# Performance work log

Hardware: AMD Instinct MI355X
Metric: run time of the kernel (lower is better)

The kernel has to match this reference:

```python
import jax, jax.numpy as jnp
import numpy as np

H, DH, DM = 8, 128, 1024          # n_head, d_head, d_model (n_head*d_head == d_model)
SLEN, BSZ = 256, 64               # slen <= 256 forced by pi0[:, :l]
SCALE = 1.0 / DH ** 0.5
LN_EPS = 1e-5


def setup_inputs() -> dict:
    key = jax.random.key(0)
    k0, k1, k2, k3 = jax.random.split(key, 4)
    h = jax.random.normal(k0, (SLEN, BSZ, DM), jnp.float32)
    W_qkv = jax.random.normal(k1, (H * 4 * DH, DM), jnp.float32) * (DM ** -0.5)
    W_o = jax.random.normal(k2, (DM, H * DH), jnp.float32) * ((H * DH) ** -0.5)
    pi0 = jax.random.uniform(k3, (H, 256), jnp.float32)
    ln_gamma = jnp.ones((DM,), jnp.float32)
    ln_beta = jnp.zeros((DM,), jnp.float32)
    return {"h": h, "W_qkv": W_qkv, "W_o": W_o, "pi0": pi0,
            "ln_gamma": ln_gamma, "ln_beta": ln_beta}


def _phi(x):
    # elu(x)+1 feature map, then L1-normalize over the feature dim
    x = jax.nn.elu(x) + 1.0
    return x / jnp.sum(x, axis=-1, keepdims=True)


def _causal_linear_attn(q, k, v):
    # fast_weight_sum: out_t = sum_{s<=t} (q_t . k_s) v_s  (zero initial fast weights)
    # q,k,v: [b,h,l,d]
    l = q.shape[2]
    scores = jnp.einsum('bhld,bhsd->bhls', q, k)
    mask = jnp.tril(jnp.ones((l, l), dtype=bool))
    scores = jnp.where(mask, scores, jnp.zeros((), scores.dtype))
    return jnp.einsum('bhls,bhsd->bhld', scores, v)


def reference(h, W_qkv, W_o, pi0, ln_gamma, ln_beta):
    l, b, _ = h.shape
    # qkv projection: [l,b,H,4*DH] -> q, k1, k2, v (update_mode='rbf2keys')
    qkv = jnp.einsum('lbm,nm->lbn', h, W_qkv).reshape(l, b, H, 4 * DH)
    q, k1, k2, v = jnp.split(qkv, 4, axis=-1)
    # permute to [b, H, l, d]
    q = _phi(jnp.transpose(q, (1, 2, 0, 3)))
    k1 = _phi(jnp.transpose(k1, (1, 2, 0, 3)))
    k2 = _phi(jnp.transpose(k2, (1, 2, 0, 3)))
    v = jnp.transpose(v, (1, 2, 0, 3))
    # two fast-weight sums (skip_attn_normalization=True path)
    lo1 = _causal_linear_attn(q, k1, v)
    lo2 = _causal_linear_attn(q, k2, v)
    pi = jnp.clip(pi0, 0.0, 1.0)[None, :, :l, None]          # [1,H,l,1]
    layer_out = SCALE * (lo1 * pi + lo2 * (1.0 - pi))         # [b,H,l,d]
    # [b,H,l,d] -> [l,b,H*d]
    layer_out = jnp.transpose(layer_out, (2, 0, 1, 3)).reshape(l, b, H * DH)
    attn_out = jnp.einsum('lbn,mn->lbm', layer_out, W_o)
    # post-LN residual (pre_lnorm=False, dropout=0)
    x = h + attn_out
    mu = jnp.mean(x, axis=-1, keepdims=True)
    var = jnp.mean((x - mu) ** 2, axis=-1, keepdims=True)
    return ln_gamma * (x - mu) / jnp.sqrt(var + LN_EPS) + ln_beta
```

## Files before the change

kernel.cpp:

```cpp
#include <hip/hip_runtime.h>

#define H_     8
#define DM_    1024
#define NQKV_  4096
#define ROWS_  16384
#define PAIRS_ 512
#define SCALE_ 0.08838834764831845f
#define LN_EPS_ 1e-5f

typedef __attribute__((ext_vector_type(8))) short short8;
typedef __attribute__((ext_vector_type(4))) float floatx4;

__device__ __forceinline__ float b2f(unsigned short u) {
  union { unsigned int i; float f; } v; v.i = ((unsigned int)u) << 16; return v.f;
}
__device__ __forceinline__ unsigned short f2b(float f) {
  union { unsigned int i; float f; } v; v.f = f;
  unsigned int b = v.i;
  b += 0x7FFFu + ((b >> 16) & 1u);
  return (unsigned short)(b >> 16);
}

__device__ __forceinline__ void stage_async(const unsigned short* __restrict__ g,
                                            size_t ld, unsigned short* s, int tid) {
#pragma unroll
  for (int p = 0; p < 4; ++p) {
    int idx = p * 256 + tid;
    int r = idx >> 3, j = idx & 7;
    int cg = j ^ (r & 7);
    __builtin_amdgcn_global_load_lds(
        (const __attribute__((address_space(1))) unsigned int*)(g + (size_t)r * ld + cg * 8),
        (__attribute__((address_space(3))) unsigned int*)(s + (size_t)idx * 8),
        16, 0, 0);
  }
}
__device__ __forceinline__ short8 lds_frag(const unsigned short* s, int row, int cg) {
  return *(const short8*)(s + row * 64 + ((cg ^ (row & 7)) << 3));
}

__global__ __launch_bounds__(256) void cvt_all(const float* __restrict__ h,
                                               const float* __restrict__ wq,
                                               const float* __restrict__ wo,
                                               unsigned short* __restrict__ hb,
                                               unsigned short* __restrict__ wqb,
                                               unsigned short* __restrict__ wob) {
  int i = blockIdx.x * 256 + threadIdx.x;
  const float* src; unsigned short* dst; int off;
  if (i < 2097152)      { src = h;  dst = hb;  off = i; }
  else if (i < 2621440) { src = wq; dst = wqb; off = i - 2097152; }
  else                  { src = wo; dst = wob; off = i - 2621440; }
  const float4* s4 = (const float4*)(src + (size_t)off * 8);
  float4 v0 = s4[0], v1 = s4[1];
  union { short8 v; unsigned short u[8]; } pk;
  pk.u[0] = f2b(v0.x); pk.u[1] = f2b(v0.y); pk.u[2] = f2b(v0.z); pk.u[3] = f2b(v0.w);
  pk.u[4] = f2b(v1.x); pk.u[5] = f2b(v1.y); pk.u[6] = f2b(v1.z); pk.u[7] = f2b(v1.w);
  *(short8*)(dst + (size_t)off * 8) = pk.v;
}

__global__ __launch_bounds__(256, 2) void qkv_gemm(const unsigned short* __restrict__ A,
                                                   const unsigned short* __restrict__ B,
                                                   unsigned short* __restrict__ QKV) {
  __shared__ alignas(16) unsigned short Sh[34816];
  unsigned short* As = Sh;
  unsigned short* Bs = Sh + 8192;
  int tid = threadIdx.x;
  int lane = tid & 63, wid = tid >> 6;
  int wm = wid >> 1, wn = wid & 1;
  int quad = lane >> 4, l16 = lane & 15;
  int n0 = blockIdx.x * 256;
  int hh = n0 >> 9, part0 = (n0 >> 7) & 3;
  int bb = blockIdx.y & 63, lhalf = blockIdx.y >> 6;

  const unsigned short* Ab = A + ((size_t)(lhalf * 128) * 64 + bb) * DM_;
  const size_t lda = (size_t)64 * DM_;
  const unsigned short* Bb = B + (size_t)n0 * DM_;

  floatx4 acc[4][8];
#pragma unroll
  for (int i = 0; i < 4; ++i)
#pragma unroll
    for (int j = 0; j < 8; ++j)
#pragma unroll
      for (int r = 0; r < 4; ++r) acc[i][j][r] = 0.f;

  for (int kt = 0; kt < DM_; kt += 64) {
    stage_async(Ab + kt, lda, As, tid);
    stage_async(Bb + kt, DM_, Bs, tid);
    stage_async(Bb + (size_t)128 * DM_ + kt, DM_, Bs + 8192, tid);
    __syncthreads();
#pragma unroll
    for (int kk = 0; kk < 2; ++kk) {
      short8 af[4], bfv[8];
#pragma unroll
      for (int mt = 0; mt < 4; ++mt)
        af[mt] = lds_frag(As, wm * 64 + mt * 16 + l16, kk * 4 + quad);
#pragma unroll
      for (int nt = 0; nt < 8; ++nt)
        bfv[nt] = lds_frag(Bs, wn * 128 + nt * 16 + l16, kk * 4 + quad);
#pragma unroll
      for (int mt = 0; mt < 4; ++mt)
#pragma unroll
        for (int nt = 0; nt < 8; ++nt)
          acc[mt][nt] = __builtin_amdgcn_mfma_f32_16x16x32_bf16(af[mt], bfv[nt], acc[mt][nt], 0, 0, 0);
    }
    __syncthreads();
  }

  int mypart = part0 + wn;
  unsigned short* T = Sh + wn * 17408;
  if (mypart < 3) {
    float rsum[4][4];
#pragma unroll
    for (int mt = 0; mt < 4; ++mt)
#pragma unroll
      for (int r = 0; r < 4; ++r) rsum[mt][r] = 0.f;
#pragma unroll
    for (int mt = 0; mt < 4; ++mt)
#pragma unroll
      for (int nt = 0; nt < 8; ++nt)
#pragma unroll
        for (int r = 0; r < 4; ++r) {
          float x = acc[mt][nt][r];
          float f = x > 0.f ? x + 1.f : __expf(x);
          acc[mt][nt][r] = f;
          rsum[mt][r] += f;
        }
#pragma unroll
    for (int off = 1; off < 16; off <<= 1)
#pragma unroll
      for (int mt = 0; mt < 4; ++mt)
#pragma unroll
        for (int r = 0; r < 4; ++r)
          rsum[mt][r] += __shfl_xor(rsum[mt][r], off);
#pragma unroll
    for (int mt = 0; mt < 4; ++mt)
#pragma unroll
      for (int r = 0; r < 4; ++r) {
        float inv = 1.f / rsum[mt][r];
        int rl = wm * 64 + mt * 16 + quad * 4 + r;
#pragma unroll
        for (int nt = 0; nt < 8; ++nt)
          T[rl * 136 + nt * 16 + l16] = f2b(acc[mt][nt][r] * inv);
      }
  } else {
#pragma unroll
    for (int mt = 0; mt < 4; ++mt)
#pragma unroll
      for (int nt = 0; nt < 8; ++nt)
#pragma unroll
        for (int r = 0; r < 4; ++r) {
          int l = wm * 64 + mt * 16 + quad * 4 + r;
          int d = nt * 16 + l16;
          T[d * 136 + l] = f2b(acc[mt][nt][r]);
        }
  }
  __syncthreads();

  int c = tid & 15, g = tid >> 4;
#pragma unroll
  for (int half = 0; half < 2; ++half) {
    int part = part0 + half;
    const unsigned short* Th = Sh + half * 17408;
    if (part < 3) {
      unsigned short* P = QKV + (size_t)part * 16777216;
      size_t base = ((size_t)((bb * 8 + hh) * 256 + lhalf * 128)) * 128;
#pragma unroll
      for (int j = 0; j < 8; ++j) {
        int rr = j * 16 + g;
        *(short8*)(P + base + rr * 128 + c * 8) = *(const short8*)(Th + rr * 136 + c * 8);
      }
    } else {
      unsigned short* Vt = QKV + (size_t)3 * 16777216;
#pragma unroll
      for (int j = 0; j < 8; ++j) {
        int d = j * 16 + g;
        size_t gb = ((size_t)((bb * 8 + hh) * 128 + d)) * 256 + lhalf * 128 + c * 8;
        *(short8*)(Vt + gb) = *(const short8*)(Th + d * 136 + c * 8);
      }
    }
  }
}

__global__ __launch_bounds__(256) void scores_kernel(const unsigned short* __restrict__ QKV,
                                                     const float* __restrict__ pi0,
                                                     unsigned short* __restrict__ S) {
  __shared__ alignas(16) unsigned short Sh[24576];
  __shared__ float pis[128];
  unsigned short* As  = Sh;
  unsigned short* Bs1 = Sh + 8192;
  unsigned short* Bs2 = Sh + 16384;
  int p = blockIdx.z;
  int hh = p & 7;
  int tid = threadIdx.x;
  int lane = tid & 63, wid = tid >> 6;
  int wm = wid >> 1, wn = wid & 1;
  int quad = lane >> 4, l16 = lane & 15;
  int tix = blockIdx.x;
  int m0 = (tix >= 1) ? 128 : 0;
  int n0 = (tix == 2) ? 128 : 0;
  if (tid < 128) {
    float pv = pi0[hh * 256 + m0 + tid];
    pis[tid] = fminf(fmaxf(pv, 0.f), 1.f);
  }
  const unsigned short* Qb  = QKV + (size_t)p * 32768 + (size_t)m0 * 128;
  const unsigned short* K1b = QKV + 16777216     + (size_t)p * 32768 + (size_t)n0 * 128;
  const unsigned short* K2b = QKV + 2 * 16777216 + (size_t)p * 32768 + (size_t)n0 * 128;

  floatx4 acc1[4][4], acc2[4][4];
#pragma unroll
  for (int i = 0; i < 4; ++i)
#pragma unroll
    for (int j = 0; j < 4; ++j)
#pragma unroll
      for (int r = 0; r < 4; ++r) { acc1[i][j][r] = 0.f; acc2[i][j][r] = 0.f; }

  for (int kt = 0; kt < 128; kt += 64) {
    stage_async(Qb + kt, 128, As, tid);
    stage_async(K1b + kt, 128, Bs1, tid);
    stage_async(K2b + kt, 128, Bs2, tid);
    __syncthreads();
#pragma unroll
    for (int kk = 0; kk < 2; ++kk) {
      short8 af[4], b1[4], b2v[4];
#pragma unroll
      for (int mt = 0; mt < 4; ++mt)
        af[mt] = lds_frag(As, wm * 64 + mt * 16 + l16, kk * 4 + quad);
#pragma unroll
      for (int nt = 0; nt < 4; ++nt) {
        b1[nt]  = lds_frag(Bs1, wn * 64 + nt * 16 + l16, kk * 4 + quad);
        b2v[nt] = lds_frag(Bs2, wn * 64 + nt * 16 + l16, kk * 4 + quad);
      }
#pragma unroll
      for (int mt = 0; mt < 4; ++mt)
#pragma unroll
        for (int nt = 0; nt < 4; ++nt) {
          acc1[mt][nt] = __builtin_amdgcn_mfma_f32_16x16x32_bf16(af[mt], b1[nt],  acc1[mt][nt], 0, 0, 0);
          acc2[mt][nt] = __builtin_amdgcn_mfma_f32_16x16x32_bf16(af[mt], b2v[nt], acc2[mt][nt], 0, 0, 0);
        }
    }
    __syncthreads();
  }
#pragma unroll
  for (int mt = 0; mt < 4; ++mt)
#pragma unroll
    for (int nt = 0; nt < 4; ++nt)
#pragma unroll
      for (int r = 0; r < 4; ++r) {
        int tl = wm * 64 + mt * 16 + quad * 4 + r;
        int sl = wn * 64 + nt * 16 + l16;
        float pv = pis[tl];
        float v = (n0 + sl <= m0 + tl) ? (pv * acc1[mt][nt][r] + (1.f - pv) * acc2[mt][nt][r]) : 0.f;
        Sh[tl * 136 + sl] = f2b(v);
      }
  __syncthreads();
  int c = tid & 15, g = tid >> 4;
#pragma unroll
  for (int j = 0; j < 8; ++j) {
    int r = j * 16 + g;
    size_t gb = (size_t)p * 65536 + (size_t)(m0 + r) * 256 + n0 + c * 8;
    *(short8*)(S + gb) = *(const short8*)(Sh + r * 136 + c * 8);
  }
}

__global__ __launch_bounds__(256, 4) void pv_kernel(const unsigned short* __restrict__ S,
                                                    const unsigned short* __restrict__ Vt,
                                                    unsigned short* __restrict__ LO) {
  __shared__ alignas(16) unsigned short Sh[17408];
  unsigned short* As = Sh;
  unsigned short* Bs = Sh + 8192;
  int p = blockIdx.z;
  int b = p >> 3, hh = p & 7;
  int tid = threadIdx.x;
  int lane = tid & 63, wid = tid >> 6;
  int wm = wid >> 1, wn = wid & 1;
  int quad = lane >> 4, l16 = lane & 15;
  int m0 = blockIdx.y * 128;
  int kEnd = (blockIdx.y == 0) ? 128 : 256;
  const unsigned short* Ab = S  + (size_t)p * 65536 + (size_t)m0 * 256;
  const unsigned short* Bb = Vt + (size_t)p * 32768;

  floatx4 acc[4][4];
#pragma unroll
  for (int i = 0; i < 4; ++i)
#pragma unroll
    for (int j = 0; j < 4; ++j)
#pragma unroll
      for (int r = 0; r < 4; ++r) acc[i][j][r] = 0.f;

  for (int kt = 0; kt < kEnd; kt += 64) {
    stage_async(Ab + kt, 256, As, tid);
    stage_async(Bb + kt, 256, Bs, tid);
    __syncthreads();
#pragma unroll
    for (int kk = 0; kk < 2; ++kk) {
      short8 af[4], bfv[4];
#pragma unroll
      for (int mt = 0; mt < 4; ++mt)
        af[mt] = lds_frag(As, wm * 64 + mt * 16 + l16, kk * 4 + quad);
#pragma unroll
      for (int nt = 0; nt < 4; ++nt)
        bfv[nt] = lds_frag(Bs, wn * 64 + nt * 16 + l16, kk * 4 + quad);
#pragma unroll
      for (int mt = 0; mt < 4; ++mt)
#pragma unroll
        for (int nt = 0; nt < 4; ++nt)
          acc[mt][nt] = __builtin_amdgcn_mfma_f32_16x16x32_bf16(af[mt], bfv[nt], acc[mt][nt], 0, 0, 0);
    }
    __syncthreads();
  }
#pragma unroll
  for (int mt = 0; mt < 4; ++mt)
#pragma unroll
    for (int nt = 0; nt < 4; ++nt)
#pragma unroll
      for (int r = 0; r < 4; ++r) {
        int tl = wm * 64 + mt * 16 + quad * 4 + r;
        int d = wn * 64 + nt * 16 + l16;
        Sh[tl * 136 + d] = f2b(SCALE_ * acc[mt][nt][r]);
      }
  __syncthreads();
  int c = tid & 15, g = tid >> 4;
#pragma unroll
  for (int j = 0; j < 8; ++j) {
    int r = j * 16 + g;
    int t = m0 + r;
    size_t gb = ((size_t)t * 64 + b) * 1024 + hh * 128 + c * 8;
    *(short8*)(LO + gb) = *(const short8*)(Sh + r * 136 + c * 8);
  }
}

__global__ __launch_bounds__(256, 4) void wo_gemm(const unsigned short* __restrict__ A,
                                                  const unsigned short* __restrict__ B,
                                                  const float* __restrict__ hin,
                                                  float* __restrict__ X) {
  __shared__ alignas(16) unsigned short As[128 * 64], Bs[128 * 64];
  int tid = threadIdx.x;
  int lane = tid & 63, wid = tid >> 6;
  int wm = wid >> 1, wn = wid & 1;
  int quad = lane >> 4, l16 = lane & 15;
  int m0 = blockIdx.y * 128, n0 = blockIdx.x * 128;
  const unsigned short* Ab = A + (size_t)m0 * DM_;
  const unsigned short* Bb = B + (size_t)n0 * DM_;

  floatx4 acc[4][4];
#pragma unroll
  for (int i = 0; i < 4; ++i)
#pragma unroll
    for (int j = 0; j < 4; ++j)
#pragma unroll
      for (int r = 0; r < 4; ++r) acc[i][j][r] = 0.f;

  for (int kt = 0; kt < DM_; kt += 64) {
    stage_async(Ab + kt, DM_, As, tid);
    stage_async(Bb + kt, DM_, Bs, tid);
    __syncthreads();
#pragma unroll
    for (int kk = 0; kk < 2; ++kk) {
      short8 af[4], bfv[4];
#pragma unroll
      for (int mt = 0; mt < 4; ++mt)
        af[mt] = lds_frag(As, wm * 64 + mt * 16 + l16, kk * 4 + quad);
#pragma unroll
      for (int nt = 0; nt < 4; ++nt)
        bfv[nt] = lds_frag(Bs, wn * 64 + nt * 16 + l16, kk * 4 + quad);
#pragma unroll
      for (int mt = 0; mt < 4; ++mt)
#pragma unroll
        for (int nt = 0; nt < 4; ++nt)
          acc[mt][nt] = __builtin_amdgcn_mfma_f32_16x16x32_bf16(af[mt], bfv[nt], acc[mt][nt], 0, 0, 0);
    }
    __syncthreads();
  }
#pragma unroll
  for (int mt = 0; mt < 4; ++mt)
#pragma unroll
    for (int nt = 0; nt < 4; ++nt)
#pragma unroll
      for (int r = 0; r < 4; ++r) {
        int row = m0 + wm * 64 + mt * 16 + quad * 4 + r;
        int col = n0 + wn * 64 + nt * 16 + l16;
        size_t idx = (size_t)row * DM_ + col;
        X[idx] = acc[mt][nt][r] + hin[idx];
      }
}

__global__ __launch_bounds__(256) void ln_kernel(float* __restrict__ X,
                                                 const float* __restrict__ gamma,
                                                 const float* __restrict__ beta) {
  int row = blockIdx.x;
  int tid = threadIdx.x;
  float* x = X + (size_t)row * DM_;
  float4 v = *(const float4*)(x + tid * 4);
  float s  = v.x + v.y + v.z + v.w;
  float ss = v.x * v.x + v.y * v.y + v.z * v.z + v.w * v.w;
#pragma unroll
  for (int off = 32; off; off >>= 1) {
    s  += __shfl_down(s, off);
    ss += __shfl_down(ss, off);
  }
  __shared__ float rs[4], rss[4];
  int wv = tid >> 6, lane = tid & 63;
  if (lane == 0) { rs[wv] = s; rss[wv] = ss; }
  __syncthreads();
  float St  = rs[0] + rs[1] + rs[2] + rs[3];
  float SSt = rss[0] + rss[1] + rss[2] + rss[3];
  float mu = St * (1.f / DM_);
  float var = SSt * (1.f / DM_) - mu * mu;
  float rstd = rsqrtf(var + LN_EPS_);
  float4 o;
#pragma unroll
  for (int j = 0; j < 4; ++j) {
    int c = tid * 4 + j;
    (&o.x)[j] = gamma[c] * ((&v.x)[j] - mu) * rstd + beta[c];
  }
  *(float4*)(x + tid * 4) = o;
}

extern "C" void kernel_launch(void* const* d_in, const int* in_sizes, int n_in,
                              void* d_out, int out_size, void* d_ws, size_t ws_size,
                              hipStream_t stream) {
  const float* h     = (const float*)d_in[0];
  const float* Wqkv  = (const float*)d_in[1];
  const float* Wo    = (const float*)d_in[2];
  const float* pi0   = (const float*)d_in[3];
  const float* gamma = (const float*)d_in[4];
  const float* beta  = (const float*)d_in[5];
  char* ws = (char*)d_ws;

  unsigned short* QKV   = (unsigned short*)ws;
  unsigned short* Sbuf  = (unsigned short*)(ws + 134217728ull);
  unsigned short* hb    = (unsigned short*)(ws + 134217728ull);
  unsigned short* Wqkvb = (unsigned short*)(ws + 167772160ull);
  unsigned short* Wob   = (unsigned short*)(ws + 201326592ull);
  unsigned short* LO    = (unsigned short*)ws;
  float* X = (float*)d_out;

  dim3 blk(256);
  cvt_all<<<dim3(10752), blk, 0, stream>>>(h, Wqkv, Wo, hb, Wqkvb, Wob);
  qkv_gemm<<<dim3(NQKV_ / 256, ROWS_ / 128, 1), blk, 0, stream>>>(hb, Wqkvb, QKV);
  scores_kernel<<<dim3(3, 1, PAIRS_), blk, 0, stream>>>(QKV, pi0, Sbuf);
  pv_kernel<<<dim3(1, 2, PAIRS_), blk, 0, stream>>>(Sbuf, QKV + (size_t)3 * 16777216, LO);
  wo_gemm<<<dim3(DM_ / 128, ROWS_ / 128, 1), blk, 0, stream>>>(LO, Wob, h, X);
  ln_kernel<<<dim3(ROWS_, 1, 1), blk, 0, stream>>>(X, gamma, beta);
}
```

Measured before the change: 466.0 us.

## Rewrite QKV GEMM as 256x256 double-buffered 8-wave pipelined kernel

The QKV projection GEMM moves from 128x256 tiles with 4 waves and a single LDS buffer to 256x256 tiles with 8 waves. Two LDS stages are used, with async prefetch of k-tile t+2 interleaved between MFMA phases and s_setprio raised around the MFMA bursts. A block-index swizzle is added for L2 locality. The epilogue is reworked so the feature-map row sums are combined across wave pairs through LDS. The aim is to hide global-load latency and raise MFMA utilization, at the cost of 128KB of LDS, more registers and many barriers.

```diff
diff --git a/kernel.cpp b/kernel.cpp
--- a/kernel.cpp
+++ b/kernel.cpp
@@ -26,6 +26,19 @@
 #pragma unroll
   for (int p = 0; p < 4; ++p) {
     int idx = p * 256 + tid;
+    int r = idx >> 3, j = idx & 7;
+    int cg = j ^ (r & 7);
+    __builtin_amdgcn_global_load_lds(
+        (const __attribute__((address_space(1))) unsigned int*)(g + (size_t)r * ld + cg * 8),
+        (__attribute__((address_space(3))) unsigned int*)(s + (size_t)idx * 8),
+        16, 0, 0);
+  }
+}
+__device__ __forceinline__ void stage_half(const unsigned short* __restrict__ g,
+                                           size_t ld, unsigned short* s, int tid) {
+#pragma unroll
+  for (int p = 0; p < 2; ++p) {
+    int idx = p * 512 + tid;
     int r = idx >> 3, j = idx & 7;
     int cg = j ^ (r & 7);
     __builtin_amdgcn_global_load_lds(
@@ -57,67 +70,149 @@
   *(short8*)(dst + (size_t)off * 8) = pk.v;
 }
 
-__global__ __launch_bounds__(256, 2) void qkv_gemm(const unsigned short* __restrict__ A,
+__global__ __launch_bounds__(512, 2) void qkv_gemm(const unsigned short* __restrict__ A,
                                                    const unsigned short* __restrict__ B,
                                                    unsigned short* __restrict__ QKV) {
-  __shared__ alignas(16) unsigned short Sh[34816];
-  unsigned short* As = Sh;
-  unsigned short* Bs = Sh + 8192;
+  __shared__ alignas(16) unsigned short Sh[65536];
   int tid = threadIdx.x;
   int lane = tid & 63, wid = tid >> 6;
-  int wm = wid >> 1, wn = wid & 1;
+  int wm = wid >> 2, wn = wid & 3;
   int quad = lane >> 4, l16 = lane & 15;
-  int n0 = blockIdx.x * 256;
-  int hh = n0 >> 9, part0 = (n0 >> 7) & 3;
-  int bb = blockIdx.y & 63, lhalf = blockIdx.y >> 6;
-
-  const unsigned short* Ab = A + ((size_t)(lhalf * 128) * 64 + bb) * DM_;
+
+  int bid = blockIdx.y * 16 + blockIdx.x;
+  int swz = (bid & 7) * 128 + (bid >> 3);
+  int bx = swz & 15, by = swz >> 4;
+  int n0 = bx * 256, hh = bx >> 1, part0 = (bx & 1) * 2, bb = by;
+
+  const unsigned short* Ab = A + (size_t)bb * DM_;
   const size_t lda = (size_t)64 * DM_;
   const unsigned short* Bb = B + (size_t)n0 * DM_;
 
-  floatx4 acc[4][8];
-#pragma unroll
-  for (int i = 0; i < 4; ++i)
-#pragma unroll
-    for (int j = 0; j < 8; ++j)
+  floatx4 acc[8][4];
+#pragma unroll
+  for (int i = 0; i < 8; ++i)
+#pragma unroll
+    for (int j = 0; j < 4; ++j)
 #pragma unroll
       for (int r = 0; r < 4; ++r) acc[i][j][r] = 0.f;
 
-  for (int kt = 0; kt < DM_; kt += 64) {
-    stage_async(Ab + kt, lda, As, tid);
-    stage_async(Bb + kt, DM_, Bs, tid);
-    stage_async(Bb + (size_t)128 * DM_ + kt, DM_, Bs + 8192, tid);
-    __syncthreads();
-#pragma unroll
-    for (int kk = 0; kk < 2; ++kk) {
-      short8 af[4], bfv[8];
-#pragma unroll
-      for (int mt = 0; mt < 4; ++mt)
-        af[mt] = lds_frag(As, wm * 64 + mt * 16 + l16, kk * 4 + quad);
-#pragma unroll
-      for (int nt = 0; nt < 8; ++nt)
-        bfv[nt] = lds_frag(Bs, wn * 128 + nt * 16 + l16, kk * 4 + quad);
-#pragma unroll
-      for (int mt = 0; mt < 4; ++mt)
-#pragma unroll
-        for (int nt = 0; nt < 8; ++nt)
-          acc[mt][nt] = __builtin_amdgcn_mfma_f32_16x16x32_bf16(af[mt], bfv[nt], acc[mt][nt], 0, 0, 0);
-    }
-    __syncthreads();
-  }
-
-  int mypart = part0 + wn;
-  unsigned short* T = Sh + wn * 17408;
-  if (mypart < 3) {
-    float rsum[4][4];
-#pragma unroll
-    for (int mt = 0; mt < 4; ++mt)
+  stage_half(Ab,                           lda, Sh,         tid);
+  stage_half(Ab + (size_t)128 * lda,       lda, Sh + 8192,  tid);
+  stage_half(Bb,                           DM_, Sh + 16384, tid);
+  stage_half(Bb + (size_t)128 * DM_,       DM_, Sh + 24576, tid);
+  stage_half(Ab + 64,                      lda, Sh + 32768, tid);
+  stage_half(Ab + (size_t)128 * lda + 64,  lda, Sh + 40960, tid);
+  stage_half(Bb + 64,                      DM_, Sh + 49152, tid);
+  stage_half(Bb + (size_t)128 * DM_ + 64,  DM_, Sh + 57344, tid);
+  asm volatile("s_waitcnt vmcnt(8)" ::: "memory");
+  __builtin_amdgcn_s_barrier();
+
+  for (int t = 0; t < 16; ++t) {
+    unsigned short* SA = Sh + (t & 1) * 32768;
+    unsigned short* SB = SA + 16384;
+    short8 a[8], b0[4], b1[4];
+
+#pragma unroll
+    for (int m = 0; m < 4; ++m)
+#pragma unroll
+      for (int kk = 0; kk < 2; ++kk)
+        a[m * 2 + kk] = lds_frag(SA, wm * 128 + m * 16 + l16, kk * 4 + quad);
+#pragma unroll
+    for (int n = 0; n < 2; ++n)
+#pragma unroll
+      for (int kk = 0; kk < 2; ++kk)
+        b0[n * 2 + kk] = lds_frag(SB, wn * 64 + n * 16 + l16, kk * 4 + quad);
+    __builtin_amdgcn_s_barrier();
+    asm volatile("s_waitcnt lgkmcnt(0)" ::: "memory");
+    __builtin_amdgcn_s_setprio(1);
+#pragma unroll
+    for (int m = 0; m < 4; ++m)
+#pragma unroll
+      for (int n = 0; n < 2; ++n)
+#pragma unroll
+        for (int kk = 0; kk < 2; ++kk)
+          acc[m][n] = __builtin_amdgcn_mfma_f32_16x16x32_bf16(a[m * 2 + kk], b0[n * 2 + kk], acc[m][n], 0, 0, 0);
+    __builtin_amdgcn_s_setprio(0);
+    __builtin_amdgcn_s_barrier();
+
+#pragma unroll
+    for (int n = 0; n < 2; ++n)
+#pragma unroll
+      for (int kk = 0; kk < 2; ++kk)
+        b1[n * 2 + kk] = lds_frag(SB, wn * 64 + 32 + n * 16 + l16, kk * 4 + quad);
+    __builtin_amdgcn_s_barrier();
+    asm volatile("s_waitcnt lgkmcnt(0)" ::: "memory");
+    __builtin_amdgcn_s_setprio(1);
+#pragma unroll
+    for (int m = 0; m < 4; ++m)
+#pragma unroll
+      for (int n = 0; n < 2; ++n)
+#pragma unroll
+        for (int kk = 0; kk < 2; ++kk)
+          acc[m][2 + n] = __builtin_amdgcn_mfma_f32_16x16x32_bf16(a[m * 2 + kk], b1[n * 2 + kk], acc[m][2 + n], 0, 0, 0);
+    __builtin_amdgcn_s_setprio(0);
+    __builtin_amdgcn_s_barrier();
+
+#pragma unroll
+    for (int m = 0; m < 4; ++m)
+#pragma unroll
+      for (int kk = 0; kk < 2; ++kk)
+        a[m * 2 + kk] = lds_frag(SA, wm * 128 + 64 + m * 16 + l16, kk * 4 + quad);
+    if (t < 14) {
+      size_t kt2 = (size_t)(t + 2) * 64;
+      stage_half(Bb + kt2,                      DM_, SB,        tid);
+      stage_half(Bb + (size_t)128 * DM_ + kt2,  DM_, SB + 8192, tid);
+    }
+    __builtin_amdgcn_s_barrier();
+    asm volatile("s_waitcnt lgkmcnt(0)" ::: "memory");
+    __builtin_amdgcn_s_setprio(1);
+#pragma unroll
+    for (int m = 0; m < 4; ++m)
+#pragma unroll
+      for (int n = 0; n < 2; ++n)
+#pragma unroll
+        for (int kk = 0; kk < 2; ++kk)
+          acc[4 + m][n] = __builtin_amdgcn_mfma_f32_16x16x32_bf16(a[m * 2 + kk], b0[n * 2 + kk], acc[4 + m][n], 0, 0, 0);
+    __builtin_amdgcn_s_setprio(0);
+    __builtin_amdgcn_s_barrier();
+
+    if (t < 14) {
+      size_t kt2 = (size_t)(t + 2) * 64;
+      stage_half(Ab + kt2,                      lda, SA,        tid);
+      stage_half(Ab + (size_t)128 * lda + kt2,  lda, SA + 8192, tid);
+    }
+    __builtin_amdgcn_s_barrier();
+    __builtin_amdgcn_s_setprio(1);
+#pragma unroll
+    for (int m = 0; m < 4; ++m)
+#pragma unroll
+      for (int n = 0; n < 2; ++n)
+#pragma unroll
+        for (int kk = 0; kk < 2; ++kk)
+          acc[4 + m][2 + n] = __builtin_amdgcn_mfma_f32_16x16x32_bf16(a[m * 2 + kk], b1[n * 2 + kk], acc[4 + m][2 + n], 0, 0, 0);
+    __builtin_amdgcn_s_setprio(0);
+    if (t < 14) {
+      asm volatile("s_waitcnt vmcnt(8)" ::: "memory");
+    } else {
+      asm volatile("s_waitcnt vmcnt(0)" ::: "memory");
+    }
+    __builtin_amdgcn_s_barrier();
+  }
+
+  __syncthreads();
+  bool isV = (part0 + (wn >> 1)) == 3;
+  float* Pf = (float*)Sh;
+  float rsum[8][4];
+  float inv[8][4];
+  if (!isV) {
+#pragma unroll
+    for (int mt = 0; mt < 8; ++mt)
 #pragma unroll
       for (int r = 0; r < 4; ++r) rsum[mt][r] = 0.f;
 #pragma unroll
-    for (int mt = 0; mt < 4; ++mt)
-#pragma unroll
-      for (int nt = 0; nt < 8; ++nt)
+    for (int mt = 0; mt < 8; ++mt)
+#pragma unroll
+      for (int nt = 0; nt < 4; ++nt)
 #pragma unroll
         for (int r = 0; r < 4; ++r) {
           float x = acc[mt][nt][r];
@@ -128,56 +223,75 @@
 #pragma unroll
     for (int off = 1; off < 16; off <<= 1)
 #pragma unroll
-      for (int mt = 0; mt < 4; ++mt)
+      for (int mt = 0; mt < 8; ++mt)
 #pragma unroll
         for (int r = 0; r < 4; ++r)
           rsum[mt][r] += __shfl_xor(rsum[mt][r], off);
-#pragma unroll
-    for (int mt = 0; mt < 4; ++mt)
-#pragma unroll
-      for (int r = 0; r < 4; ++r) {
-        float inv = 1.f / rsum[mt][r];
-        int rl = wm * 64 + mt * 16 + quad * 4 + r;
-#pragma unroll
-        for (int nt = 0; nt < 8; ++nt)
-          T[rl * 136 + nt * 16 + l16] = f2b(acc[mt][nt][r] * inv);
-      }
-  } else {
-#pragma unroll
-    for (int mt = 0; mt < 4; ++mt)
-#pragma unroll
-      for (int nt = 0; nt < 8; ++nt)
-#pragma unroll
-        for (int r = 0; r < 4; ++r) {
-          int l = wm * 64 + mt * 16 + quad * 4 + r;
-          int d = nt * 16 + l16;
-          T[d * 136 + l] = f2b(acc[mt][nt][r]);
-        }
+    if (l16 == 0) {
+#pragma unroll
+      for (int mt = 0; mt < 8; ++mt)
+#pragma unroll
+        for (int r = 0; r < 4; ++r)
+          Pf[(wm * 128 + mt * 16 + quad * 4 + r) * 4 + wn] = rsum[mt][r];
+    }
   }
   __syncthreads();
-
-  int c = tid & 15, g = tid >> 4;
-#pragma unroll
-  for (int half = 0; half < 2; ++half) {
-    int part = part0 + half;
-    const unsigned short* Th = Sh + half * 17408;
+  if (!isV) {
+#pragma unroll
+    for (int mt = 0; mt < 8; ++mt)
+#pragma unroll
+      for (int r = 0; r < 4; ++r)
+        inv[mt][r] = 1.f / (rsum[mt][r] + Pf[(wm * 128 + mt * 16 + quad * 4 + r) * 4 + (wn ^ 1)]);
+  }
+  __syncthreads();
+
+#pragma unroll
+  for (int h = 0; h < 2; ++h) {
+    int part = part0 + h;
+    if ((wn >> 1) == h) {
+      if (part < 3) {
+#pragma unroll
+        for (int mt = 0; mt < 8; ++mt)
+#pragma unroll
+          for (int nt = 0; nt < 4; ++nt)
+#pragma unroll
+            for (int r = 0; r < 4; ++r) {
+              int row = wm * 128 + mt * 16 + quad * 4 + r;
+              int col = (wn & 1) * 64 + nt * 16 + l16;
+              Sh[row * 136 + col] = f2b(acc[mt][nt][r] * inv[mt][r]);
+            }
+      } else {
+#pragma unroll
+        for (int mt = 0; mt < 8; ++mt)
+#pragma unroll
+          for (int nt = 0; nt < 4; ++nt)
+#pragma unroll
+            for (int r = 0; r < 4; ++r) {
+              int d = (wn & 1) * 64 + nt * 16 + l16;
+              int l = wm * 128 + mt * 16 + quad * 4 + r;
+              Sh[d * 264 + l] = f2b(acc[mt][nt][r]);
+            }
+      }
+    }
+    __syncthreads();
     if (part < 3) {
-      unsigned short* P = QKV + (size_t)part * 16777216;
-      size_t base = ((size_t)((bb * 8 + hh) * 256 + lhalf * 128)) * 128;
+      unsigned short* P = QKV + (size_t)part * 16777216 + (size_t)(bb * 8 + hh) * 32768;
+      int c = tid & 15, g = tid >> 4;
 #pragma unroll
       for (int j = 0; j < 8; ++j) {
-        int rr = j * 16 + g;
-        *(short8*)(P + base + rr * 128 + c * 8) = *(const short8*)(Th + rr * 136 + c * 8);
+        int row = j * 32 + g;
+        *(short8*)(P + (size_t)row * 128 + c * 8) = *(const short8*)(Sh + row * 136 + c * 8);
       }
     } else {
-      unsigned short* Vt = QKV + (size_t)3 * 16777216;
+      unsigned short* Vt = QKV + (size_t)3 * 16777216 + (size_t)(bb * 8 + hh) * 32768;
+      int cg = tid & 31, g = tid >> 5;
 #pragma unroll
       for (int j = 0; j < 8; ++j) {
         int d = j * 16 + g;
-        size_t gb = ((size_t)((bb * 8 + hh) * 128 + d)) * 256 + lhalf * 128 + c * 8;
-        *(short8*)(Vt + gb) = *(const short8*)(Th + d * 136 + c * 8);
-      }
-    }
+        *(short8*)(Vt + (size_t)d * 256 + cg * 8) = *(const short8*)(Sh + d * 264 + cg * 8);
+      }
+    }
+    __syncthreads();
   }
 }
 
@@ -437,7 +551,7 @@
 
   dim3 blk(256);
   cvt_all<<<dim3(10752), blk, 0, stream>>>(h, Wqkv, Wo, hb, Wqkvb, Wob);
-  qkv_gemm<<<dim3(NQKV_ / 256, ROWS_ / 128, 1), blk, 0, stream>>>(hb, Wqkvb, QKV);
+  qkv_gemm<<<dim3(16, 64, 1), dim3(512), 0, stream>>>(hb, Wqkvb, QKV);
   scores_kernel<<<dim3(3, 1, PAIRS_), blk, 0, stream>>>(QKV, pi0, Sbuf);
   pv_kernel<<<dim3(1, 2, PAIRS_), blk, 0, stream>>>(Sbuf, QKV + (size_t)3 * 16777216, LO);
   wo_gemm<<<dim3(DM_ / 128, ROWS_ / 128, 1), blk, 0, stream>>>(LO, Wob, h, X);
```

New measurement: 445.0 us. 1.05x faster.

## Shrink QKV GEMM tile to 128x128, swizzle block order, raise occupancy

Applied to the files above, without the earlier changes.

Cuts the QKV projection tile from 128x256 to 128x128 so shared memory per block halves and launch bounds allow four blocks per CU. The feature-map row sum is now split across two waves and combined through shared memory. A block-index swizzle is added so that consecutive blocks share operand tiles, which should improve L2 reuse. The cost is reloading each A tile twice as often, lower MFMA work per LDS fragment load, and extra barriers in the epilogue.

```diff
diff --git a/kernel.cpp b/kernel.cpp
--- a/kernel.cpp
+++ b/kernel.cpp
@@ -57,58 +57,60 @@
   *(short8*)(dst + (size_t)off * 8) = pk.v;
 }
 
-__global__ __launch_bounds__(256, 2) void qkv_gemm(const unsigned short* __restrict__ A,
+__global__ __launch_bounds__(256, 4) void qkv_gemm(const unsigned short* __restrict__ A,
                                                    const unsigned short* __restrict__ B,
                                                    unsigned short* __restrict__ QKV) {
-  __shared__ alignas(16) unsigned short Sh[34816];
+  __shared__ alignas(16) unsigned short Sh[17408];
   unsigned short* As = Sh;
   unsigned short* Bs = Sh + 8192;
   int tid = threadIdx.x;
   int lane = tid & 63, wid = tid >> 6;
   int wm = wid >> 1, wn = wid & 1;
   int quad = lane >> 4, l16 = lane & 15;
-  int n0 = blockIdx.x * 256;
-  int hh = n0 >> 9, part0 = (n0 >> 7) & 3;
-  int bb = blockIdx.y & 63, lhalf = blockIdx.y >> 6;
+
+  int bid = blockIdx.y * 32 + blockIdx.x;
+  int swz = (bid & 7) * 512 + (bid >> 3);
+  int bx = swz & 31, by = swz >> 5;
+  int n0 = bx * 128;
+  int part = bx & 3, hh = bx >> 2;
+  int bb = by & 63, lhalf = by >> 6;
 
   const unsigned short* Ab = A + ((size_t)(lhalf * 128) * 64 + bb) * DM_;
   const size_t lda = (size_t)64 * DM_;
   const unsigned short* Bb = B + (size_t)n0 * DM_;
 
-  floatx4 acc[4][8];
+  floatx4 acc[4][4];
 #pragma unroll
   for (int i = 0; i < 4; ++i)
 #pragma unroll
-    for (int j = 0; j < 8; ++j)
+    for (int j = 0; j < 4; ++j)
 #pragma unroll
       for (int r = 0; r < 4; ++r) acc[i][j][r] = 0.f;
 
   for (int kt = 0; kt < DM_; kt += 64) {
     stage_async(Ab + kt, lda, As, tid);
     stage_async(Bb + kt, DM_, Bs, tid);
-    stage_async(Bb + (size_t)128 * DM_ + kt, DM_, Bs + 8192, tid);
     __syncthreads();
 #pragma unroll
     for (int kk = 0; kk < 2; ++kk) {
-      short8 af[4], bfv[8];
+      short8 af[4], bfv[4];
 #pragma unroll
       for (int mt = 0; mt < 4; ++mt)
         af[mt] = lds_frag(As, wm * 64 + mt * 16 + l16, kk * 4 + quad);
 #pragma unroll
-      for (int nt = 0; nt < 8; ++nt)
-        bfv[nt] = lds_frag(Bs, wn * 128 + nt * 16 + l16, kk * 4 + quad);
-#pragma unroll
-      for (int mt = 0; mt < 4; ++mt)
-#pragma unroll
-        for (int nt = 0; nt < 8; ++nt)
+      for (int nt = 0; nt < 4; ++nt)
+        bfv[nt] = lds_frag(Bs, wn * 64 + nt * 16 + l16, kk * 4 + quad);
+#pragma unroll
+      for (int mt = 0; mt < 4; ++mt)
+#pragma unroll
+        for (int nt = 0; nt < 4; ++nt)
           acc[mt][nt] = __builtin_amdgcn_mfma_f32_16x16x32_bf16(af[mt], bfv[nt], acc[mt][nt], 0, 0, 0);
     }
     __syncthreads();
   }
 
-  int mypart = part0 + wn;
-  unsigned short* T = Sh + wn * 17408;
-  if (mypart < 3) {
+  int c = tid & 15, g = tid >> 4;
+  if (part < 3) {
     float rsum[4][4];
 #pragma unroll
     for (int mt = 0; mt < 4; ++mt)
@@ -117,7 +119,7 @@
 #pragma unroll
     for (int mt = 0; mt < 4; ++mt)
 #pragma unroll
-      for (int nt = 0; nt < 8; ++nt)
+      for (int nt = 0; nt < 4; ++nt)
 #pragma unroll
         for (int r = 0; r < 4; ++r) {
           float x = acc[mt][nt][r];
@@ -132,51 +134,57 @@
 #pragma unroll
         for (int r = 0; r < 4; ++r)
           rsum[mt][r] += __shfl_xor(rsum[mt][r], off);
+    float* Pf = (float*)Sh;
+    if (l16 == 0) {
+#pragma unroll
+      for (int mt = 0; mt < 4; ++mt)
+#pragma unroll
+        for (int r = 0; r < 4; ++r)
+          Pf[(wm * 64 + mt * 16 + quad * 4 + r) * 2 + wn] = rsum[mt][r];
+    }
+    __syncthreads();
+    float inv[4][4];
 #pragma unroll
     for (int mt = 0; mt < 4; ++mt)
 #pragma unroll
-      for (int r = 0; r < 4; ++r) {
-        float inv = 1.f / rsum[mt][r];
-        int rl = wm * 64 + mt * 16 + quad * 4 + r;
-#pragma unroll
-        for (int nt = 0; nt < 8; ++nt)
-          T[rl * 136 + nt * 16 + l16] = f2b(acc[mt][nt][r] * inv);
-      }
+      for (int r = 0; r < 4; ++r)
+        inv[mt][r] = 1.f / (rsum[mt][r] + Pf[(wm * 64 + mt * 16 + quad * 4 + r) * 2 + (wn ^ 1)]);
+    __syncthreads();
+#pragma unroll
+    for (int mt = 0; mt < 4; ++mt)
+#pragma unroll
+      for (int nt = 0; nt < 4; ++nt)
+#pragma unroll
+        for (int r = 0; r < 4; ++r) {
+          int row = wm * 64 + mt * 16 + quad * 4 + r;
+          int col = wn * 64 + nt * 16 + l16;
+          Sh[row * 136 + col] = f2b(acc[mt][nt][r] * inv[mt][r]);
+        }
+    __syncthreads();
+    unsigned short* P = QKV + (size_t)part * 16777216 + (size_t)(bb * 8 + hh) * 32768
+                            + (size_t)(lhalf * 128) * 128;
+#pragma unroll
+    for (int j = 0; j < 8; ++j) {
+      int row = j * 16 + g;
+      *(short8*)(P + (size_t)row * 128 + c * 8) = *(const short8*)(Sh + row * 136 + c * 8);
+    }
   } else {
 #pragma unroll
     for (int mt = 0; mt < 4; ++mt)
 #pragma unroll
-      for (int nt = 0; nt < 8; ++nt)
+      for (int nt = 0; nt < 4; ++nt)
 #pragma unroll
         for (int r = 0; r < 4; ++r) {
           int l = wm * 64 + mt * 16 + quad * 4 + r;
-          int d = nt * 16 + l16;
-          T[d * 136 + l] = f2b(acc[mt][nt][r]);
+          int d = wn * 64 + nt * 16 + l16;
+          Sh[d * 136 + l] = f2b(acc[mt][nt][r]);
         }
-  }
-  __syncthreads();
-
-  int c = tid & 15, g = tid >> 4;
-#pragma unroll
-  for (int half = 0; half < 2; ++half) {
-    int part = part0 + half;
-    const unsigned short* Th = Sh + half * 17408;
-    if (part < 3) {
-      unsigned short* P = QKV + (size_t)part * 16777216;
-      size_t base = ((size_t)((bb * 8 + hh) * 256 + lhalf * 128)) * 128;
-#pragma unroll
-      for (int j = 0; j < 8; ++j) {
-        int rr = j * 16 + g;
-        *(short8*)(P + base + rr * 128 + c * 8) = *(const short8*)(Th + rr * 136 + c * 8);
-      }
-    } else {
-      unsigned short* Vt = QKV + (size_t)3 * 16777216;
-#pragma unroll
-      for (int j = 0; j < 8; ++j) {
-        int d = j * 16 + g;
-        size_t gb = ((size_t)((bb * 8 + hh) * 128 + d)) * 256 + lhalf * 128 + c * 8;
-        *(short8*)(Vt + gb) = *(const short8*)(Th + d * 136 + c * 8);
-      }
+    __syncthreads();
+    unsigned short* Vt = QKV + (size_t)3 * 16777216 + (size_t)(bb * 8 + hh) * 32768;
+#pragma unroll
+    for (int j = 0; j < 8; ++j) {
+      int d = j * 16 + g;
+      *(short8*)(Vt + (size_t)d * 256 + lhalf * 128 + c * 8) = *(const short8*)(Sh + d * 136 + c * 8);
     }
   }
 }
@@ -437,7 +445,7 @@
 
   dim3 blk(256);
   cvt_all<<<dim3(10752), blk, 0, stream>>>(h, Wqkv, Wo, hb, Wqkvb, Wob);
-  qkv_gemm<<<dim3(NQKV_ / 256, ROWS_ / 128, 1), blk, 0, stream>>>(hb, Wqkvb, QKV);
+  qkv_gemm<<<dim3(32, 128, 1), blk, 0, stream>>>(hb, Wqkvb, QKV);
   scores_kernel<<<dim3(3, 1, PAIRS_), blk, 0, stream>>>(QKV, pi0, Sbuf);
   pv_kernel<<<dim3(1, 2, PAIRS_), blk, 0, stream>>>(Sbuf, QKV + (size_t)3 * 16777216, LO);
   wo_gemm<<<dim3(DM_ / 128, ROWS_ / 128, 1), blk, 0, stream>>>(LO, Wob, h, X);
```

Result: slower. 515.5 us (+10.6%).
